# Kernel tuning notes

Hardware: AMD Instinct MI355X
Metric: run time of the kernel (lower is better)

The kernel has to match this reference:

```python
import jax, jax.numpy as jnp
import numpy as np

N, E, F, H, G, C = 50000, 800000, 768, 256, 512, 2  # H = nhid*2 (nhid=128), G graphs, C classes
NHID = 128


def setup_inputs() -> dict:
    key = jax.random.key(0)
    ks = jax.random.split(key, 18)
    s = 0.05
    x = jax.random.normal(ks[0], (N, F), jnp.float32)
    edge_index = jax.random.randint(ks[1], (2, E), 0, N, dtype=jnp.int32)
    # sorted batch vector; every graph non-empty so the 'first node per graph' gather is valid
    batch = ((jnp.arange(N) * G) // N).astype(jnp.int32)
    return {
        "x": x,
        "edge_index": edge_index,
        "batch": batch,
        # GATConv 1 (in=F, out=H, heads=1)
        "W1": jax.random.normal(ks[2], (F, H), jnp.float32) * s,
        "as1": jax.random.normal(ks[3], (H,), jnp.float32) * s,
        "ad1": jax.random.normal(ks[4], (H,), jnp.float32) * s,
        "b1": jnp.zeros((H,), jnp.float32),
        # GATConv 2 (in=H, out=H)
        "W2": jax.random.normal(ks[5], (H, H), jnp.float32) * s,
        "as2": jax.random.normal(ks[6], (H,), jnp.float32) * s,
        "ad2": jax.random.normal(ks[7], (H,), jnp.float32) * s,
        "b2": jnp.zeros((H,), jnp.float32),
        # fc0: num_features -> nhid (news branch)
        "W0": jax.random.normal(ks[8], (F, NHID), jnp.float32) * s,
        "b0": jnp.zeros((NHID,), jnp.float32),
        # fc1: 2*nhid -> nhid (used twice, as in the source)
        "Wf1": jax.random.normal(ks[9], (H, NHID), jnp.float32) * s,
        "bf1": jnp.zeros((NHID,), jnp.float32),
        # fc2: nhid -> num_classes
        "Wf2": jax.random.normal(ks[10], (NHID, C), jnp.float32) * s,
        "bf2": jnp.zeros((C,), jnp.float32),
    }


def _gat(x, src, dst, W, a_s, a_d, b):
    # PyG GATConv, heads=1, concat=True, negative_slope=0.2, self-loops pre-appended to src/dst.
    h = x @ W                                   # [N, H]
    e = jax.nn.leaky_relu((h @ a_s)[src] + (h @ a_d)[dst], 0.2)  # [E+N]
    m = jax.ops.segment_max(e, dst, num_segments=N)
    ex = jnp.exp(e - m[dst])                    # stable segment softmax numerator
    denom = jax.ops.segment_sum(ex, dst, num_segments=N)
    agg = jax.ops.segment_sum(ex[:, None] * h[src], dst, num_segments=N)  # [N, H]
    return agg / denom[:, None] + b


def reference(x, edge_index, batch, W1, as1, ad1, b1, W2, as2, ad2, b2, W0, b0, Wf1, bf1, Wf2, bf2):
    loop = jnp.arange(N, dtype=edge_index.dtype)
    src = jnp.concatenate([edge_index[0], loop])  # add self-loops (PyG default)
    dst = jnp.concatenate([edge_index[1], loop])
    h = jax.nn.selu(_gat(x, src, dst, W1, as1, ad1, b1))
    h = jax.nn.selu(_gat(h, src, dst, W2, as2, ad2, b2))
    # global mean pool over graphs
    cnt = jax.ops.segment_sum(jnp.ones((N,), h.dtype), batch, num_segments=G)
    pooled = jax.nn.selu(jax.ops.segment_sum(h, batch, num_segments=G) / cnt[:, None])
    z = jax.nn.selu(pooled @ Wf1 + bf1)
    # dropout(p=0.5) in eval mode -> identity
    # concat branch: first node of each graph (news root)
    first_idx = jax.ops.segment_min(jnp.arange(N), batch, num_segments=G)
    news = jax.nn.relu(x[first_idx] @ W0 + b0)
    z = jnp.concatenate([z, news], axis=1)       # [G, 2*nhid]
    z = jax.nn.relu(z @ Wf1 + bf1)
    return jax.nn.log_softmax(z @ Wf2 + bf2, axis=-1)
```

## Files before the change

### kernel.cpp

```cpp
#include <hip/hip_runtime.h>
#include <hip/hip_bf16.h>
#include <cstdint>
#include <cstddef>

#define NN 50000
#define EE 800000
#define FF 768
#define HH 256
#define GG 512
#define CC 2
#define NHIDD 128
#define ETOT (EE + NN)
#define NCHUNK 49

typedef __attribute__((ext_vector_type(8))) short bf16x8;
typedef __attribute__((ext_vector_type(4))) float f32x4;
typedef __attribute__((ext_vector_type(8))) unsigned short us8;

__device__ __forceinline__ float b2f(unsigned short u){
  union { float f; uint32_t i; } v; v.i = ((uint32_t)u) << 16; return v.f;
}
__device__ __forceinline__ unsigned short f2b(float f){
  uint32_t u = __float_as_uint(f);
  uint32_t r = (u + 0x7fffu + ((u >> 16) & 1u)) >> 16;
  return (unsigned short)r;
}
__device__ __forceinline__ float selu_f(float x){
  const float lam = 1.0507009873554805f, alp = 1.6732632423543772f;
  return x > 0.f ? lam * x : lam * alp * (__expf(x) - 1.f);
}

__device__ __forceinline__ void gload_lds16(const unsigned short* g, unsigned short* l){
  __builtin_amdgcn_global_load_lds((const __attribute__((address_space(1))) void*)g,
                                   (__attribute__((address_space(3))) void*)l, 16, 0, 0);
}

__global__ __launch_bounds__(256) void xbf_kernel(const float* __restrict__ x, unsigned short* __restrict__ xb){
  size_t i = ((size_t)blockIdx.x * 256 + threadIdx.x) * 8;
  float4 f0 = *(const float4*)&x[i];
  float4 f1 = *(const float4*)&x[i + 4];
  us8 v;
  v[0] = f2b(f0.x); v[1] = f2b(f0.y); v[2] = f2b(f0.z); v[3] = f2b(f0.w);
  v[4] = f2b(f1.x); v[5] = f2b(f1.y); v[6] = f2b(f1.z); v[7] = f2b(f1.w);
  *(us8*)&xb[i] = v;
}

__global__ __launch_bounds__(256) void swizzleW(const float* __restrict__ W,
                                                unsigned short* __restrict__ Wsw, int K){
  int i = blockIdx.x * 256 + threadIdx.x;
  if (i < K * HH){
    int k = i / HH, n = i % HH;
    Wsw[(size_t)(k >> 5) * 8192 + n * 32 + (k & 31)] = f2b(W[i]);
  }
}

__global__ __launch_bounds__(256) void zero_deg(int* deg){
  int i = blockIdx.x * 256 + threadIdx.x;
  if (i < NN) deg[i] = 0;
}

__global__ __launch_bounds__(256) void deg_kernel(const int* __restrict__ dstA, int* __restrict__ deg){
  int i = blockIdx.x * 256 + threadIdx.x;
  if (i < ETOT){
    int d = (i < EE) ? dstA[i] : (i - EE);
    atomicAdd(&deg[d], 1);
  }
}

__global__ __launch_bounds__(256) void scanA(const int* __restrict__ deg, int* __restrict__ bsum){
  __shared__ int red[256];
  int c = blockIdx.x, tid = threadIdx.x;
  int base = c * 1024 + tid * 4;
  int s = 0;
#pragma unroll
  for (int j = 0; j < 4; j++){ int idx = base + j; if (idx < NN) s += deg[idx]; }
  red[tid] = s; __syncthreads();
  for (int off = 128; off > 0; off >>= 1){
    if (tid < off) red[tid] += red[tid + off];
    __syncthreads();
  }
  if (tid == 0) bsum[c] = red[0];
}

__global__ __launch_bounds__(256) void scanC(const int* __restrict__ deg, const int* __restrict__ bsum,
                                             int* __restrict__ row_ptr, int* __restrict__ fill_ptr){
  __shared__ int ts[256];
  __shared__ int cbase;
  int c = blockIdx.x, tid = threadIdx.x;
  int pb = (tid < c) ? bsum[tid] : 0;
  ts[tid] = pb; __syncthreads();
  for (int off = 128; off > 0; off >>= 1){
    if (tid < off) ts[tid] += ts[tid + off];
    __syncthreads();
  }
  if (tid == 0) cbase = ts[0];
  __syncthreads();
  int base = c * 1024 + tid * 4;
  int v[4]; int s = 0;
#pragma unroll
  for (int j = 0; j < 4; j++){ int idx = base + j; v[j] = (idx < NN) ? deg[idx] : 0; s += v[j]; }
  ts[tid] = s; __syncthreads();
  for (int off = 1; off < 256; off <<= 1){
    int add = (tid >= off) ? ts[tid - off] : 0;
    __syncthreads();
    ts[tid] += add;
    __syncthreads();
  }
  int run = ts[tid] - s + cbase;
#pragma unroll
  for (int j = 0; j < 4; j++){
    int idx = base + j;
    if (idx < NN){ row_ptr[idx] = run; fill_ptr[idx] = run; }
    run += v[j];
  }
  if (c == 0 && tid == 0) row_ptr[NN] = ETOT;
}

__global__ __launch_bounds__(256) void fill_kernel(const int* __restrict__ srcA, const int* __restrict__ dstA,
                                                   int* __restrict__ fill_ptr, int* __restrict__ csr_src){
  int i = blockIdx.x * 256 + threadIdx.x;
  if (i < ETOT){
    int s = (i < EE) ? srcA[i] : (i - EE);
    int d = (i < EE) ? dstA[i] : (i - EE);
    int pos = atomicAdd(&fill_ptr[d], 1);
    csr_src[pos] = s;
  }
}

template<int K, int MINW>
__global__ __launch_bounds__(256, MINW) void gemm_mfma(const unsigned short* __restrict__ A,
                                                 const unsigned short* __restrict__ Wsw,
                                                 const float* __restrict__ a_s, const float* __restrict__ a_d,
                                                 unsigned short* __restrict__ out,
                                                 float* __restrict__ als, float* __restrict__ ald, int M){
  constexpr int CHROW = K / 8;
  __shared__ unsigned short Al[32 * K];
  const int tid = threadIdx.x;
  const int m0 = blockIdx.x * 32;
  const int lane = tid & 63, w = tid >> 6;
  const int koff = (lane >> 4) * 8;
  const int arow = lane & 15;
  const int nrow = w * 64 + (lane & 15);

  f32x4 acc[2][4];
#pragma unroll
  for (int rt = 0; rt < 2; rt++)
#pragma unroll
    for (int ct = 0; ct < 4; ct++) acc[rt][ct] = (f32x4){0.f, 0.f, 0.f, 0.f};

  constexpr int ROUNDS = (32 * CHROW) / 256;
#pragma unroll
  for (int j = 0; j < ROUNDS; j++){
    int L16 = j * 256 + tid;
    int row = L16 / CHROW;
    int ch  = L16 - row * CHROW;
    int sch = ch ^ (row & 7);
    int gr  = m0 + row; if (gr >= M) gr = M - 1;
    gload_lds16(A + (size_t)gr * K + sch * 8,
                &Al[(size_t)(j * 256 + w * 64) * 8]);
  }

  const unsigned short* bbase = Wsw + ((size_t)nrow * 32 + koff);
  bf16x8 bcur[2][4];
#pragma unroll
  for (int k2 = 0; k2 < 2; k2++)
#pragma unroll
    for (int ct = 0; ct < 4; ct++)
      bcur[k2][ct] = *(const bf16x8*)(bbase + (size_t)k2 * 8192 + ct * 512);

  __syncthreads();

  constexpr int NIT = K / 64;
  for (int ks = 0; ks < NIT; ks++){
    bf16x8 bnext[2][4];
    if (ks + 1 < NIT){
#pragma unroll
      for (int k2 = 0; k2 < 2; k2++)
#pragma unroll
        for (int ct = 0; ct < 4; ct++)
          bnext[k2][ct] = *(const bf16x8*)(bbase + (size_t)((ks + 1) * 2 + k2) * 8192 + ct * 512);
    }
    bf16x8 af[2][2];
#pragma unroll
    for (int k2 = 0; k2 < 2; k2++)
#pragma unroll
      for (int rt = 0; rt < 2; rt++){
        int R = rt * 16 + arow;
        int chb = (ks * 8 + k2 * 4 + (lane >> 4)) ^ (R & 7);
        af[k2][rt] = *(const bf16x8*)&Al[(size_t)R * K + chb * 8];
      }
#pragma unroll
    for (int k2 = 0; k2 < 2; k2++)
#pragma unroll
      for (int rt = 0; rt < 2; rt++)
#pragma unroll
        for (int ct = 0; ct < 4; ct++)
          acc[rt][ct] = __builtin_amdgcn_mfma_f32_16x16x32_bf16(af[k2][rt], bcur[k2][ct], acc[rt][ct], 0, 0, 0);
    if (ks + 1 < NIT){
#pragma unroll
      for (int k2 = 0; k2 < 2; k2++)
#pragma unroll
        for (int ct = 0; ct < 4; ct++) bcur[k2][ct] = bnext[k2][ct];
    }
  }

#pragma unroll
  for (int rt = 0; rt < 2; rt++){
    int mbase = m0 + rt * 16 + (lane >> 4) * 4;
#pragma unroll
    for (int r = 0; r < 4; r++){
      int m = mbase + r;
      if (m < M){
        size_t ro = (size_t)m * HH + w * 64 + (lane & 15);
        out[ro + 0]  = f2b(acc[rt][0][r]);
        out[ro + 16] = f2b(acc[rt][1][r]);
        out[ro + 32] = f2b(acc[rt][2][r]);
        out[ro + 48] = f2b(acc[rt][3][r]);
      }
    }
  }

  float as_c[4], ad_c[4];
#pragma unroll
  for (int ct = 0; ct < 4; ct++){
    int col = w * 64 + ct * 16 + (lane & 15);
    as_c[ct] = a_s[col]; ad_c[ct] = a_d[col];
  }
  float ps[2][4], pd[2][4];
#pragma unroll
  for (int rt = 0; rt < 2; rt++)
#pragma unroll
    for (int r = 0; r < 4; r++){
      float s = 0.f, d = 0.f;
#pragma unroll
      for (int ct = 0; ct < 4; ct++){ float v = acc[rt][ct][r]; s += v * as_c[ct]; d += v * ad_c[ct]; }
      ps[rt][r] = s; pd[rt][r] = d;
    }
#pragma unroll
  for (int off = 1; off < 16; off <<= 1){
#pragma unroll
    for (int rt = 0; rt < 2; rt++)
#pragma unroll
      for (int r = 0; r < 4; r++){
        ps[rt][r] += __shfl_xor(ps[rt][r], off);
        pd[rt][r] += __shfl_xor(pd[rt][r], off);
      }
  }
  __syncthreads();
  float* red = (float*)Al;
  if ((lane & 15) == 0){
    int q = lane >> 4;
#pragma unroll
    for (int rt = 0; rt < 2; rt++)
#pragma unroll
      for (int r = 0; r < 4; r++){
        int row = rt * 16 + q * 4 + r;
        red[w * 32 + row]       = ps[rt][r];
        red[128 + w * 32 + row] = pd[rt][r];
      }
  }
  __syncthreads();
  if (tid < 32){
    float s = red[tid] + red[32 + tid] + red[64 + tid] + red[96 + tid];
    float d = red[128 + tid] + red[160 + tid] + red[192 + tid] + red[224 + tid];
    int m = m0 + tid;
    if (m < M){ als[m] = s; ald[m] = d; }
  }
}

__global__ __launch_bounds__(256) void agg_wave(const unsigned short* __restrict__ h,
    const float* __restrict__ als, const float* __restrict__ ald,
    const int* __restrict__ row_ptr, const int* __restrict__ csr_src,
    const float* __restrict__ bias, unsigned short* __restrict__ outp){
  int node = blockIdx.x * 4 + (threadIdx.x >> 6);
  int lane = threadIdx.x & 63;
  if (node >= NN) return;
  int base = row_ptr[node];
  int deg  = row_ptr[node + 1] - base;
  float aldd = ald[node];
  float den = 0.f;
  float a[8] = {0.f, 0.f, 0.f, 0.f, 0.f, 0.f, 0.f, 0.f};
  const int f8 = (lane & 31) * 8;
  const int half = lane >> 5;
  for (int p0 = 0; p0 < deg; p0 += 64){
    int cnt = min(64, deg - p0);
    float ev = 0.f; int s = 0;
    if (lane < cnt){
      s = csr_src[base + p0 + lane];
      float v = als[s] + aldd;
      v = v > 0.f ? v : 0.2f * v;
      ev = __expf(v);
    }
    den += ev;
    int j = 0;
    for (; j + 4 <= cnt; j += 4){
      int j0 = j + half, j1 = j + 2 + half;
      int s0 = __shfl(s, j0), s1 = __shfl(s, j1);
      float e0 = __shfl(ev, j0), e1 = __shfl(ev, j1);
      us8 g0 = *(const us8*)&h[(size_t)s0 * HH + f8];
      us8 g1 = *(const us8*)&h[(size_t)s1 * HH + f8];
#pragma unroll
      for (int i = 0; i < 8; i++) a[i] += e0 * b2f(g0[i]) + e1 * b2f(g1[i]);
    }
    for (; j < cnt; j += 2){
      int jj = j + half;
      int sj = __shfl(s, jj & 63);
      float ejr = __shfl(ev, jj & 63);
      float ej = (jj < cnt) ? ejr : 0.f;
      us8 gj = *(const us8*)&h[(size_t)sj * HH + f8];
#pragma unroll
      for (int i = 0; i < 8; i++) a[i] += ej * b2f(gj[i]);
    }
  }
  for (int off = 32; off > 0; off >>= 1) den += __shfl_xor(den, off);
#pragma unroll
  for (int i = 0; i < 8; i++) a[i] += __shfl_xor(a[i], 32);
  if (lane < 32){
    float inv = 1.f / den;
    float4 b4a = *(const float4*)&bias[f8];
    float4 b4b = *(const float4*)&bias[f8 + 4];
    us8 o;
    o[0] = f2b(selu_f(a[0] * inv + b4a.x));
    o[1] = f2b(selu_f(a[1] * inv + b4a.y));
    o[2] = f2b(selu_f(a[2] * inv + b4a.z));
    o[3] = f2b(selu_f(a[3] * inv + b4a.w));
    o[4] = f2b(selu_f(a[4] * inv + b4b.x));
    o[5] = f2b(selu_f(a[5] * inv + b4b.y));
    o[6] = f2b(selu_f(a[6] * inv + b4b.z));
    o[7] = f2b(selu_f(a[7] * inv + b4b.w));
    *(us8*)&outp[(size_t)node * HH + f8] = o;
  }
}

__global__ __launch_bounds__(256) void head_kernel(const unsigned short* __restrict__ x3,
    const int* __restrict__ batch, const float* __restrict__ x,
    const float* __restrict__ W0, const float* __restrict__ b0,
    const float* __restrict__ Wf1, const float* __restrict__ bf1,
    const float* __restrict__ Wf2, const float* __restrict__ bf2,
    float* __restrict__ out){
  __shared__ float pr[HH];
  __shared__ float xr[FF];
  __shared__ float zc[HH];
  __shared__ int se[2];
  __shared__ float l0s[2], l1s[2];
  int g = blockIdx.x, t = threadIdx.x;
  if (t < 2){
    int target = g + t, lo = 0, hi = NN;
    while (lo < hi){ int mid = (lo + hi) >> 1; if (batch[mid] < target) lo = mid + 1; else hi = mid; }
    se[t] = lo;
  }
  __syncthreads();
  int s = se[0], e = se[1];
  {
    float acc = 0.f;
    for (int n = s; n < e; n++) acc += b2f(x3[(size_t)n * HH + t]);
    pr[t] = selu_f(acc / (float)(e - s));
  }
  for (int k = t; k < FF; k += 256) xr[k] = x[(size_t)s * FF + k];
  __syncthreads();
  if (t < NHIDD){
    float acc = 0.f;
    for (int k = 0; k < HH; k++) acc += pr[k] * Wf1[k * NHIDD + t];
    zc[t] = selu_f(acc + bf1[t]);
  } else {
    int t2 = t - NHIDD;
    float acc = 0.f;
    for (int k = 0; k < FF; k++) acc += xr[k] * W0[k * NHIDD + t2];
    acc += b0[t2];
    zc[NHIDD + t2] = acc > 0.f ? acc : 0.f;
  }
  __syncthreads();
  if (t < NHIDD){
    float acc = 0.f;
    for (int k = 0; k < HH; k++) acc += zc[k] * Wf1[k * NHIDD + t];
    float z2 = acc + bf1[t]; z2 = z2 > 0.f ? z2 : 0.f;
    float p0 = z2 * Wf2[t * CC + 0];
    float p1 = z2 * Wf2[t * CC + 1];
    for (int off = 32; off > 0; off >>= 1){ p0 += __shfl_xor(p0, off); p1 += __shfl_xor(p1, off); }
    if ((t & 63) == 0){ l0s[t >> 6] = p0; l1s[t >> 6] = p1; }
  }
  __syncthreads();
  if (t == 0){
    float l0 = l0s[0] + l0s[1] + bf2[0];
    float l1 = l1s[0] + l1s[1] + bf2[1];
    float mx = fmaxf(l0, l1);
    float lse = mx + logf(__expf(l0 - mx) + __expf(l1 - mx));
    out[g * CC + 0] = l0 - lse;
    out[g * CC + 1] = l1 - lse;
  }
}

extern "C" void kernel_launch(void* const* d_in, const int* in_sizes, int n_in,
                              void* d_out, int out_size, void* d_ws, size_t ws_size,
                              hipStream_t stream){
  const float* x          = (const float*)d_in[0];
  const int* edge_index   = (const int*)d_in[1];
  const int* batch        = (const int*)d_in[2];
  const float* W1  = (const float*)d_in[3];
  const float* as1 = (const float*)d_in[4];
  const float* ad1 = (const float*)d_in[5];
  const float* b1  = (const float*)d_in[6];
  const float* W2  = (const float*)d_in[7];
  const float* as2 = (const float*)d_in[8];
  const float* ad2 = (const float*)d_in[9];
  const float* b2  = (const float*)d_in[10];
  const float* W0  = (const float*)d_in[11];
  const float* b0  = (const float*)d_in[12];
  const float* Wf1 = (const float*)d_in[13];
  const float* bf1 = (const float*)d_in[14];
  const float* Wf2 = (const float*)d_in[15];
  const float* bf2 = (const float*)d_in[16];
  float* out = (float*)d_out;

  char* w = (char*)d_ws;
  size_t off = 0;
  auto alloc = [&](size_t bytes){ size_t o = off; off += (bytes + 255) & ~(size_t)255; return o; };
  unsigned short* h    = (unsigned short*)(w + alloc((size_t)NN * HH * 2));
  unsigned short* x2   = (unsigned short*)(w + alloc((size_t)NN * HH * 2));
  unsigned short* xb   = (unsigned short*)(w + alloc((size_t)NN * FF * 2));
  unsigned short* Wsw1 = (unsigned short*)(w + alloc((size_t)FF * HH * 2));
  unsigned short* Wsw2 = (unsigned short*)(w + alloc((size_t)HH * HH * 2));
  float* als     = (float*)(w + alloc((size_t)NN * 4));
  float* ald     = (float*)(w + alloc((size_t)NN * 4));
  int*   deg     = (int*)(w + alloc((size_t)NN * 4));
  int*   row_ptr = (int*)(w + alloc((size_t)(NN + 1) * 4));
  int*   fillp   = (int*)(w + alloc((size_t)NN * 4));
  int*   csr_src = (int*)(w + alloc((size_t)ETOT * 4));
  int*   bsum    = (int*)(w + alloc(64 * 4));

  const int* srcA = edge_index;
  const int* dstA = edge_index + EE;

  swizzleW<<<(FF * HH + 255) / 256, 256, 0, stream>>>(W1, Wsw1, FF);
  swizzleW<<<(HH * HH + 255) / 256, 256, 0, stream>>>(W2, Wsw2, HH);
  xbf_kernel<<<(NN * FF) / (256 * 8), 256, 0, stream>>>(x, xb);

  zero_deg<<<(NN + 255) / 256, 256, 0, stream>>>(deg);
  deg_kernel<<<(ETOT + 255) / 256, 256, 0, stream>>>(dstA, deg);
  scanA<<<NCHUNK, 256, 0, stream>>>(deg, bsum);
  scanC<<<NCHUNK, 256, 0, stream>>>(deg, bsum, row_ptr, fillp);
  fill_kernel<<<(ETOT + 255) / 256, 256, 0, stream>>>(srcA, dstA, fillp, csr_src);

  const int gemm_grid = (NN + 31) / 32;
  gemm_mfma<FF, 3><<<gemm_grid, 256, 0, stream>>>(xb, Wsw1, as1, ad1, h, als, ald, NN);
  agg_wave<<<(NN + 3) / 4, 256, 0, stream>>>(h, als, ald, row_ptr, csr_src, b1, x2);
  gemm_mfma<HH, 3><<<gemm_grid, 256, 0, stream>>>(x2, Wsw2, as2, ad2, h, als, ald, NN);
  agg_wave<<<(NN + 3) / 4, 256, 0, stream>>>(h, als, ald, row_ptr, csr_src, b2, x2);
  head_kernel<<<GG, 256, 0, stream>>>(x2, batch, x, W0, b0, Wf1, bf1, Wf2, bf2, out);
}
```

Measured before the change: 618.0 us.

## Fuse fp32-to-bf16 conversion of x into first GEMM; merge weight swizzles

Removes the separate pass that converts x to bf16 and writes a bf16 copy. The first-layer GEMM now stages fp32 rows of x into LDS in two halves and converts them to bf16 in registers with v_cvt_pk_bf16_f32 before the MFMA. The two weight-swizzle launches are merged into one, and the aggregation inner loop gets an 8-neighbor unrolled path for more memory-level parallelism. The GEMM now reads twice as many bytes of A and uses a 48KB LDS tile with an extra barrier, which may lower occupancy.

Result: faster. 580.5 us (-6.1%).

```diff
diff --git a/kernel.cpp b/kernel.cpp
--- a/kernel.cpp
+++ b/kernel.cpp
@@ -25,32 +25,31 @@
   uint32_t r = (u + 0x7fffu + ((u >> 16) & 1u)) >> 16;
   return (unsigned short)r;
 }
+__device__ __forceinline__ uint32_t cvtpk(float a, float b){
+  uint32_t d;
+  asm volatile("v_cvt_pk_bf16_f32 %0, %1, %2" : "=v"(d) : "v"(a), "v"(b));
+  return d;
+}
 __device__ __forceinline__ float selu_f(float x){
   const float lam = 1.0507009873554805f, alp = 1.6732632423543772f;
   return x > 0.f ? lam * x : lam * alp * (__expf(x) - 1.f);
 }
 
-__device__ __forceinline__ void gload_lds16(const unsigned short* g, unsigned short* l){
+__device__ __forceinline__ void gload_lds16(const void* g, void* l){
   __builtin_amdgcn_global_load_lds((const __attribute__((address_space(1))) void*)g,
                                    (__attribute__((address_space(3))) void*)l, 16, 0, 0);
 }
 
-__global__ __launch_bounds__(256) void xbf_kernel(const float* __restrict__ x, unsigned short* __restrict__ xb){
-  size_t i = ((size_t)blockIdx.x * 256 + threadIdx.x) * 8;
-  float4 f0 = *(const float4*)&x[i];
-  float4 f1 = *(const float4*)&x[i + 4];
-  us8 v;
-  v[0] = f2b(f0.x); v[1] = f2b(f0.y); v[2] = f2b(f0.z); v[3] = f2b(f0.w);
-  v[4] = f2b(f1.x); v[5] = f2b(f1.y); v[6] = f2b(f1.z); v[7] = f2b(f1.w);
-  *(us8*)&xb[i] = v;
-}
-
-__global__ __launch_bounds__(256) void swizzleW(const float* __restrict__ W,
-                                                unsigned short* __restrict__ Wsw, int K){
+__global__ __launch_bounds__(256) void swizzleW2(const float* __restrict__ W1, const float* __restrict__ W2,
+                                                 unsigned short* __restrict__ Wsw1, unsigned short* __restrict__ Wsw2){
   int i = blockIdx.x * 256 + threadIdx.x;
-  if (i < K * HH){
+  if (i < FF * HH){
     int k = i / HH, n = i % HH;
-    Wsw[(size_t)(k >> 5) * 8192 + n * 32 + (k & 31)] = f2b(W[i]);
+    Wsw1[(size_t)(k >> 5) * 8192 + n * 32 + (k & 31)] = f2b(W1[i]);
+  } else {
+    int i2 = i - FF * HH;
+    int k = i2 / HH, n = i2 % HH;
+    Wsw2[(size_t)(k >> 5) * 8192 + n * 32 + (k & 31)] = f2b(W2[i2]);
   }
 }
 
@@ -124,6 +123,156 @@
     int d = (i < EE) ? dstA[i] : (i - EE);
     int pos = atomicAdd(&fill_ptr[d], 1);
     csr_src[pos] = s;
+  }
+}
+
+__global__ __launch_bounds__(256, 3) void gemm1_f32(const float* __restrict__ A,
+                                                 const unsigned short* __restrict__ Wsw,
+                                                 const float* __restrict__ a_s, const float* __restrict__ a_d,
+                                                 unsigned short* __restrict__ out,
+                                                 float* __restrict__ als, float* __restrict__ ald, int M){
+  __shared__ float Alf[32 * 384];
+  const int tid = threadIdx.x;
+  const int m0 = blockIdx.x * 32;
+  const int lane = tid & 63, w = tid >> 6;
+  const int koff = (lane >> 4) * 8;
+  const int arow = lane & 15;
+  const int nrow = w * 64 + (lane & 15);
+
+  f32x4 acc[2][4];
+#pragma unroll
+  for (int rt = 0; rt < 2; rt++)
+#pragma unroll
+    for (int ct = 0; ct < 4; ct++) acc[rt][ct] = (f32x4){0.f, 0.f, 0.f, 0.f};
+
+  const unsigned short* bbase = Wsw + ((size_t)nrow * 32 + koff);
+  bf16x8 bcur[2][4];
+
+  auto stage_half = [&](int p){
+#pragma unroll
+    for (int j = 0; j < 12; j++){
+      int L16 = j * 256 + tid;
+      int row = L16 / 96;
+      int ch  = L16 - row * 96;
+      int sch = ch ^ (row & 7);
+      int gr  = m0 + row; if (gr >= M) gr = M - 1;
+      gload_lds16(A + (size_t)gr * FF + p * 384 + sch * 4,
+                  Alf + (size_t)(j * 256 + w * 64) * 4);
+    }
+  };
+
+#pragma unroll
+  for (int p = 0; p < 2; p++){
+    if (p == 1) __syncthreads();
+    stage_half(p);
+#pragma unroll
+    for (int k2 = 0; k2 < 2; k2++)
+#pragma unroll
+      for (int ct = 0; ct < 4; ct++)
+        bcur[k2][ct] = *(const bf16x8*)(bbase + (size_t)(p * 12 + k2) * 8192 + ct * 512);
+    __syncthreads();
+
+    for (int ks = 0; ks < 6; ks++){
+      bf16x8 bnext[2][4];
+      if (ks + 1 < 6){
+#pragma unroll
+        for (int k2 = 0; k2 < 2; k2++)
+#pragma unroll
+          for (int ct = 0; ct < 4; ct++)
+            bnext[k2][ct] = *(const bf16x8*)(bbase + (size_t)(p * 12 + (ks + 1) * 2 + k2) * 8192 + ct * 512);
+      }
+      bf16x8 af[2][2];
+#pragma unroll
+      for (int k2 = 0; k2 < 2; k2++)
+#pragma unroll
+        for (int rt = 0; rt < 2; rt++){
+          int R = rt * 16 + arow;
+          int c = ks * 16 + k2 * 8 + (lane >> 4) * 2;
+          int m = R & 7;
+          float4 v0 = *(const float4*)&Alf[R * 384 + ((c)     ^ m) * 4];
+          float4 v1 = *(const float4*)&Alf[R * 384 + ((c + 1) ^ m) * 4];
+          union { bf16x8 v; uint32_t u[4]; } X;
+          X.u[0] = cvtpk(v0.x, v0.y); X.u[1] = cvtpk(v0.z, v0.w);
+          X.u[2] = cvtpk(v1.x, v1.y); X.u[3] = cvtpk(v1.z, v1.w);
+          af[k2][rt] = X.v;
+        }
+#pragma unroll
+      for (int k2 = 0; k2 < 2; k2++)
+#pragma unroll
+        for (int rt = 0; rt < 2; rt++)
+#pragma unroll
+          for (int ct = 0; ct < 4; ct++)
+            acc[rt][ct] = __builtin_amdgcn_mfma_f32_16x16x32_bf16(af[k2][rt], bcur[k2][ct], acc[rt][ct], 0, 0, 0);
+      if (ks + 1 < 6){
+#pragma unroll
+        for (int k2 = 0; k2 < 2; k2++)
+#pragma unroll
+          for (int ct = 0; ct < 4; ct++) bcur[k2][ct] = bnext[k2][ct];
+      }
+    }
+  }
+
+#pragma unroll
+  for (int rt = 0; rt < 2; rt++){
+    int mbase = m0 + rt * 16 + (lane >> 4) * 4;
+#pragma unroll
+    for (int r = 0; r < 4; r++){
+      int m = mbase + r;
+      if (m < M){
+        size_t ro = (size_t)m * HH + w * 64 + (lane & 15);
+        out[ro + 0]  = f2b(acc[rt][0][r]);
+        out[ro + 16] = f2b(acc[rt][1][r]);
+        out[ro + 32] = f2b(acc[rt][2][r]);
+        out[ro + 48] = f2b(acc[rt][3][r]);
+      }
+    }
+  }
+
+  float as_c[4], ad_c[4];
+#pragma unroll
+  for (int ct = 0; ct < 4; ct++){
+    int col = w * 64 + ct * 16 + (lane & 15);
+    as_c[ct] = a_s[col]; ad_c[ct] = a_d[col];
+  }
+  float ps[2][4], pd[2][4];
+#pragma unroll
+  for (int rt = 0; rt < 2; rt++)
+#pragma unroll
+    for (int r = 0; r < 4; r++){
+      float s = 0.f, d = 0.f;
+#pragma unroll
+      for (int ct = 0; ct < 4; ct++){ float v = acc[rt][ct][r]; s += v * as_c[ct]; d += v * ad_c[ct]; }
+      ps[rt][r] = s; pd[rt][r] = d;
+    }
+#pragma unroll
+  for (int off = 1; off < 16; off <<= 1){
+#pragma unroll
+    for (int rt = 0; rt < 2; rt++)
+#pragma unroll
+      for (int r = 0; r < 4; r++){
+        ps[rt][r] += __shfl_xor(ps[rt][r], off);
+        pd[rt][r] += __shfl_xor(pd[rt][r], off);
+      }
+  }
+  __syncthreads();
+  float* red = Alf;
+  if ((lane & 15) == 0){
+    int q = lane >> 4;
+#pragma unroll
+    for (int rt = 0; rt < 2; rt++)
+#pragma unroll
+      for (int r = 0; r < 4; r++){
+        int row = rt * 16 + q * 4 + r;
+        red[w * 32 + row]       = ps[rt][r];
+        red[128 + w * 32 + row] = pd[rt][r];
+      }
+  }
+  __syncthreads();
+  if (tid < 32){
+    float s = red[tid] + red[32 + tid] + red[64 + tid] + red[96 + tid];
+    float d = red[128 + tid] + red[160 + tid] + red[192 + tid] + red[224 + tid];
+    int m = m0 + tid;
+    if (m < M){ als[m] = s; ald[m] = d; }
   }
 }
 
@@ -293,6 +442,19 @@
     }
     den += ev;
     int j = 0;
+    for (; j + 8 <= cnt; j += 8){
+      int j0 = j + half, j1 = j + 2 + half, j2 = j + 4 + half, j3 = j + 6 + half;
+      int s0 = __shfl(s, j0), s1 = __shfl(s, j1), s2 = __shfl(s, j2), s3 = __shfl(s, j3);
+      float e0 = __shfl(ev, j0), e1 = __shfl(ev, j1), e2 = __shfl(ev, j2), e3 = __shfl(ev, j3);
+      us8 g0 = *(const us8*)&h[(size_t)s0 * HH + f8];
+      us8 g1 = *(const us8*)&h[(size_t)s1 * HH + f8];
+      us8 g2 = *(const us8*)&h[(size_t)s2 * HH + f8];
+      us8 g3 = *(const us8*)&h[(size_t)s3 * HH + f8];
+#pragma unroll
+      for (int i = 0; i < 8; i++) a[i] += e0 * b2f(g0[i]) + e1 * b2f(g1[i]);
+#pragma unroll
+      for (int i = 0; i < 8; i++) a[i] += e2 * b2f(g2[i]) + e3 * b2f(g3[i]);
+    }
     for (; j + 4 <= cnt; j += 4){
       int j0 = j + half, j1 = j + 2 + half;
       int s0 = __shfl(s, j0), s1 = __shfl(s, j1);
@@ -417,7 +579,6 @@
   auto alloc = [&](size_t bytes){ size_t o = off; off += (bytes + 255) & ~(size_t)255; return o; };
   unsigned short* h    = (unsigned short*)(w + alloc((size_t)NN * HH * 2));
   unsigned short* x2   = (unsigned short*)(w + alloc((size_t)NN * HH * 2));
-  unsigned short* xb   = (unsigned short*)(w + alloc((size_t)NN * FF * 2));
   unsigned short* Wsw1 = (unsigned short*)(w + alloc((size_t)FF * HH * 2));
   unsigned short* Wsw2 = (unsigned short*)(w + alloc((size_t)HH * HH * 2));
   float* als     = (float*)(w + alloc((size_t)NN * 4));
@@ -431,9 +592,7 @@
   const int* srcA = edge_index;
   const int* dstA = edge_index + EE;
 
-  swizzleW<<<(FF * HH + 255) / 256, 256, 0, stream>>>(W1, Wsw1, FF);
-  swizzleW<<<(HH * HH + 255) / 256, 256, 0, stream>>>(W2, Wsw2, HH);
-  xbf_kernel<<<(NN * FF) / (256 * 8), 256, 0, stream>>>(x, xb);
+  swizzleW2<<<(FF * HH + HH * HH) / 256, 256, 0, stream>>>(W1, W2, Wsw1, Wsw2);
 
   zero_deg<<<(NN + 255) / 256, 256, 0, stream>>>(deg);
   deg_kernel<<<(ETOT + 255) / 256, 256, 0, stream>>>(dstA, deg);
@@ -442,7 +601,7 @@
   fill_kernel<<<(ETOT + 255) / 256, 256, 0, stream>>>(srcA, dstA, fillp, csr_src);
 
   const int gemm_grid = (NN + 31) / 32;
-  gemm_mfma<FF, 3><<<gemm_grid, 256, 0, stream>>>(xb, Wsw1, as1, ad1, h, als, ald, NN);
+  gemm1_f32<<<gemm_grid, 256, 0, stream>>>(x, Wsw1, as1, ad1, h, als, ald, NN);
   agg_wave<<<(NN + 3) / 4, 256, 0, stream>>>(h, als, ald, row_ptr, csr_src, b1, x2);
   gemm_mfma<HH, 3><<<gemm_grid, 256, 0, stream>>>(x2, Wsw2, as2, ad2, h, als, ald, NN);
   agg_wave<<<(NN + 3) / 4, 256, 0, stream>>>(h, als, ald, row_ptr, csr_src, b2, x2);
```
